# Optimization experiments

Hardware: AMD Instinct MI355X
Metric: run time of the kernel (lower is better)

Reference implementation:

```python
import jax, jax.numpy as jnp
import numpy as np

N, F_IN, UNITS, HEADS = 8192, 256, 64, 4
NEG_BIG = -1e10


def setup_inputs() -> dict:
    key = jax.random.key(0)
    k1, k2, k3, k4, k5 = jax.random.split(key, 5)
    X = jax.random.normal(k1, (N, F_IN), dtype=jnp.float32)
    # sparse-ish binary adjacency with self-loops (float mask, as used by the module)
    A = (jax.random.uniform(k2, (N, N)) < 0.004).astype(jnp.float32)
    A = jnp.maximum(A, jnp.eye(N, dtype=jnp.float32))
    W = jax.random.normal(k3, (HEADS, F_IN, UNITS), dtype=jnp.float32) * (1.0 / np.sqrt(F_IN))
    attn_self = jax.random.normal(k4, (HEADS, UNITS), dtype=jnp.float32) * (1.0 / np.sqrt(UNITS))
    attn_neigh = jax.random.normal(k5, (HEADS, UNITS), dtype=jnp.float32) * (1.0 / np.sqrt(UNITS))
    return {"X": X, "A": A, "W": W, "attn_self": attn_self, "attn_neigh": attn_neigh}


def reference(X, A, W, attn_self, attn_neigh):
    # per-head linear projection: [H, N, U]
    feats = jnp.einsum('nf,hfu->hnu', X, W)
    a_self = jnp.einsum('hnu,hu->hn', feats, attn_self)    # [H, N]
    a_neigh = jnp.einsum('hnu,hu->hn', feats, attn_neigh)  # [H, N]
    # additive GAT scores: e_ij = a_self_i + a_neigh_j -> [H, N, N]
    scores = a_self[:, :, None] + a_neigh[:, None, :]
    scores = jax.nn.leaky_relu(scores, negative_slope=0.2)
    scores = scores + NEG_BIG * (1.0 - A)  # additive mask on non-edges
    attn = jax.nn.softmax(scores, axis=-1)
    # dropout is identity at training=False (module default)
    out = jnp.einsum('hnm,hmu->hnu', attn, feats)  # [H, N, U]
    # 'concat' reduction: head-major concat along feature dim -> [N, H*U]
    out = jnp.transpose(out, (1, 0, 2)).reshape(N, HEADS * UNITS)
    return jax.nn.elu(out)
```

## Files before the change

### kernel.cpp

```cpp
#include <hip/hip_runtime.h>

#define NN    8192
#define FIN   256
#define UNITS 64
#define HEADS 4
#define CTOT  256
#define CAP   256
#define PBLK  512

__global__ __launch_bounds__(256) void k_proj_scan(const float* __restrict__ X,
                                                   const float* __restrict__ W,
                                                   const float* __restrict__ atts,
                                                   const float* __restrict__ attn,
                                                   const float* __restrict__ A,
                                                   float* __restrict__ feats,
                                                   float* __restrict__ s_self,
                                                   float* __restrict__ s_neigh,
                                                   int*   __restrict__ ej_g,
                                                   int*   __restrict__ cnt_g) {
    const int tid = threadIdx.x;
    const int bid = blockIdx.x;

    if (bid >= PBLK) {
        __shared__ int ej[CAP];
        __shared__ int cnt;
        const int i = bid - PBLK;
        if (tid == 0) cnt = 0;
        __syncthreads();
        {
            const float4* Arow4 = reinterpret_cast<const float4*>(A + (size_t)i * NN);
            unsigned mask = 0;
            #pragma unroll
            for (int q = 0; q < 8; ++q) {
                const float4 v = Arow4[q * 256 + tid];
                mask |= (v.x != 0.f ? 1u : 0u) << (4 * q);
                mask |= (v.y != 0.f ? 1u : 0u) << (4 * q + 1);
                mask |= (v.z != 0.f ? 1u : 0u) << (4 * q + 2);
                mask |= (v.w != 0.f ? 1u : 0u) << (4 * q + 3);
            }
            const int c = __popc(mask);
            int base = 0;
            if (c) base = atomicAdd(&cnt, c);
            while (mask) {
                const int b = __ffs(mask) - 1;
                mask &= mask - 1;
                if (base < CAP) ej[base] = (b >> 2) * 1024 + tid * 4 + (b & 3);
                ++base;
            }
        }
        __syncthreads();
        const int ne = min(cnt, CAP);
        if (tid < ne) ej_g[(size_t)i * CAP + tid] = ej[tid];
        if (tid == 0) cnt_g[i] = ne;
        return;
    }

    __shared__ float Xt[32 * 68];
    __shared__ float Wl[32 * 68];
    __shared__ float reds[64];
    __shared__ float redn[64];
    const int rt = bid & 127;
    const int h  = bid >> 7;
    const int r0 = rt * 64;

    const int r  = (tid & 15) * 4;
    const int cl = (tid >> 4) * 4;
    const int srow = tid >> 2;
    const int skq  = (tid & 3) * 8;
    const int wk   = tid >> 3;
    const int wu   = (tid & 7) * 8;

    if (tid < 64) { reds[tid] = 0.f; redn[tid] = 0.f; }

    float acc[4][4];
    #pragma unroll
    for (int a = 0; a < 4; ++a)
        #pragma unroll
        for (int b = 0; b < 4; ++b) acc[a][b] = 0.f;

    for (int k0 = 0; k0 < FIN; k0 += 32) {
        __syncthreads();
        {
            const float4* xp = reinterpret_cast<const float4*>(
                X + (size_t)(r0 + srow) * FIN + k0 + skq);
            const float4 x0 = xp[0], x1 = xp[1];
            const float xs[8] = {x0.x, x0.y, x0.z, x0.w, x1.x, x1.y, x1.z, x1.w};
            #pragma unroll
            for (int m = 0; m < 8; ++m) Xt[(skq + m) * 68 + srow] = xs[m];
        }
        {
            const float4* wp = reinterpret_cast<const float4*>(
                W + (size_t)h * (FIN * UNITS) + (size_t)(k0 + wk) * UNITS + wu);
            const float4 w0 = wp[0], w1 = wp[1];
            const float ws8[8] = {w0.x, w0.y, w0.z, w0.w, w1.x, w1.y, w1.z, w1.w};
            #pragma unroll
            for (int m = 0; m < 8; ++m) Wl[wk * 68 + wu + m] = ws8[m];
        }
        __syncthreads();
        #pragma unroll 8
        for (int k = 0; k < 32; ++k) {
            const float4 a4 = *reinterpret_cast<const float4*>(&Xt[k * 68 + r]);
            const float4 b4 = *reinterpret_cast<const float4*>(&Wl[k * 68 + cl]);
            const float av[4] = {a4.x, a4.y, a4.z, a4.w};
            const float bv[4] = {b4.x, b4.y, b4.z, b4.w};
            #pragma unroll
            for (int ri = 0; ri < 4; ++ri)
                #pragma unroll
                for (int ci = 0; ci < 4; ++ci)
                    acc[ri][ci] += av[ri] * bv[ci];
        }
    }

    float as4[4], an4[4];
    #pragma unroll
    for (int ci = 0; ci < 4; ++ci) {
        as4[ci] = atts[h * UNITS + cl + ci];
        an4[ci] = attn[h * UNITS + cl + ci];
    }
    #pragma unroll
    for (int ri = 0; ri < 4; ++ri) {
        float4 o = make_float4(acc[ri][0], acc[ri][1], acc[ri][2], acc[ri][3]);
        *reinterpret_cast<float4*>(&feats[(size_t)(r0 + r + ri) * CTOT + h * UNITS + cl]) = o;
        const float ps = acc[ri][0] * as4[0] + acc[ri][1] * as4[1]
                       + acc[ri][2] * as4[2] + acc[ri][3] * as4[3];
        const float pn = acc[ri][0] * an4[0] + acc[ri][1] * an4[1]
                       + acc[ri][2] * an4[2] + acc[ri][3] * an4[3];
        atomicAdd(&reds[r + ri], ps);
        atomicAdd(&redn[r + ri], pn);
    }
    __syncthreads();
    if (tid < 64) {
        s_self [((size_t)(r0 + tid) << 2) + h] = reds[tid];
        s_neigh[((size_t)(r0 + tid) << 2) + h] = redn[tid];
    }
}

__global__ __launch_bounds__(256) void k_gat(const int*   __restrict__ ej_g,
                                             const int*   __restrict__ cnt_g,
                                             const float* __restrict__ feats,
                                             const float* __restrict__ s_self,
                                             const float* __restrict__ s_neigh,
                                             float* __restrict__ out) {
    __shared__ int   ej[CAP];
    __shared__ float sc[HEADS][CAP];
    __shared__ float part[HEADS][CTOT];
    __shared__ float rls[HEADS];
    const int tid = threadIdx.x;
    const int i   = blockIdx.x;
    const int ne  = cnt_g[i];
    if (tid < ne) ej[tid] = ej_g[(size_t)i * CAP + tid];
    __syncthreads();

    const int w    = tid >> 6;
    const int lane = tid & 63;
    const float si = s_self[((size_t)i << 2) + w];
    float m = -3.0e38f;
    for (int jj = lane; jj < ne; jj += 64) {
        const int j = ej[jj];
        float e = si + s_neigh[((size_t)j << 2) + w];
        e = (e > 0.f) ? e : 0.2f * e;
        sc[w][jj] = e;
        m = fmaxf(m, e);
    }
    #pragma unroll
    for (int off = 32; off > 0; off >>= 1) m = fmaxf(m, __shfl_xor(m, off, 64));
    float l = 0.f;
    for (int jj = lane; jj < ne; jj += 64) {
        const float p = __expf(sc[w][jj] - m);
        sc[w][jj] = p;
        l += p;
    }
    #pragma unroll
    for (int off = 32; off > 0; off >>= 1) l += __shfl_xor(l, off, 64);
    if (lane == 0) rls[w] = 1.f / l;
    __syncthreads();

    const int h4 = lane >> 4;
    float4 o = make_float4(0.f, 0.f, 0.f, 0.f);
    int jj = w;
    for (; jj + 4 < ne; jj += 8) {
        const int ja = ej[jj], jb = ej[jj + 4];
        const float pa = sc[h4][jj], pb = sc[h4][jj + 4];
        const float4 fa = *reinterpret_cast<const float4*>(
            &feats[(size_t)ja * CTOT + 4 * lane]);
        const float4 fc = *reinterpret_cast<const float4*>(
            &feats[(size_t)jb * CTOT + 4 * lane]);
        o.x += pa * fa.x + pb * fc.x;
        o.y += pa * fa.y + pb * fc.y;
        o.z += pa * fa.z + pb * fc.z;
        o.w += pa * fa.w + pb * fc.w;
    }
    if (jj < ne) {
        const int ja = ej[jj];
        const float pa = sc[h4][jj];
        const float4 fa = *reinterpret_cast<const float4*>(
            &feats[(size_t)ja * CTOT + 4 * lane]);
        o.x += pa * fa.x; o.y += pa * fa.y; o.z += pa * fa.z; o.w += pa * fa.w;
    }
    *reinterpret_cast<float4*>(&part[w][4 * lane]) = o;
    __syncthreads();

    const int c = tid;
    float s = part[0][c] + part[1][c] + part[2][c] + part[3][c];
    s *= rls[c >> 6];
    const float rr = (s > 0.f) ? s : (__expf(s) - 1.f);
    out[(size_t)i * CTOT + c] = rr;
}

extern "C" void kernel_launch(void* const* d_in, const int* in_sizes, int n_in,
                              void* d_out, int out_size, void* d_ws, size_t ws_size,
                              hipStream_t stream) {
    const float* X    = (const float*)d_in[0];
    const float* A    = (const float*)d_in[1];
    const float* W    = (const float*)d_in[2];
    const float* atts = (const float*)d_in[3];
    const float* attn = (const float*)d_in[4];

    float* feats   = (float*)d_ws;
    float* s_self  = feats  + (size_t)NN * CTOT;
    float* s_neigh = s_self + (size_t)NN * HEADS;
    int*   cnt_g   = (int*)(s_neigh + (size_t)NN * HEADS);
    int*   ej_g    = cnt_g + NN;

    k_proj_scan<<<PBLK + NN, 256, 0, stream>>>(X, W, atts, attn, A,
                                               feats, s_self, s_neigh, ej_g, cnt_g);
    k_gat<<<NN, 256, 0, stream>>>(ej_g, cnt_g, feats, s_self, s_neigh, (float*)d_out);
}
```

Measured before the change: 393.8 us.

## Fuse projection, adjacency scan and attention into one cooperative persistent kernel

Replaces the two-kernel launch with a single cooperative kernel of 1024 persistent blocks. The first 512 blocks run the projection GEMM and then scan fewer adjacency rows, while the rest scan more rows, which balances the load. A grid-wide sync follows, after which each block handles 8 rows of softmax aggregation. This removes one launch and overlaps the projection with the A scan, at the cost of a grid barrier, fewer blocks for latency hiding, and a dependence on cooperative launch residency (with the old path as fallback).

Measured after the change: 732.5 us. 86.0% more time.

```diff
diff --git a/kernel.cpp b/kernel.cpp
--- a/kernel.cpp
+++ b/kernel.cpp
@@ -1,4 +1,7 @@
 #include <hip/hip_runtime.h>
+#include <hip/hip_cooperative_groups.h>
+
+namespace cg = cooperative_groups;
 
 #define NN    8192
 #define FIN   256
@@ -6,8 +9,211 @@
 #define HEADS 4
 #define CTOT  256
 #define CAP   256
+
+#define GRID  1024
+#define GBLK  512
+#define RA1   6
+#define RA2   10
+#define RB    8
+
+__global__ __launch_bounds__(256, 4) void k_fused(
+    const float* __restrict__ X,    const float* __restrict__ W,
+    const float* __restrict__ atts, const float* __restrict__ attn,
+    const float* __restrict__ A,
+    float* __restrict__ feats, float* __restrict__ s_self, float* __restrict__ s_neigh,
+    int*   __restrict__ ej_g,  int*   __restrict__ cnt_g,
+    float* __restrict__ out)
+{
+    __shared__ float Xt[32 * 68];
+    __shared__ float Wl[32 * 68];
+    __shared__ float reds[64], redn[64];
+    __shared__ int   ej[CAP];
+    __shared__ int   cnt;
+    __shared__ float sc[HEADS][CAP];
+    __shared__ float part[HEADS][CTOT];
+    __shared__ float rls[HEADS];
+
+    const int tid = threadIdx.x;
+    const int bid = blockIdx.x;
+
+    if (bid < GBLK) {
+        const int rt = bid & 127;
+        const int h  = bid >> 7;
+        const int r0 = rt * 64;
+
+        const int r  = (tid & 15) * 4;
+        const int cl = (tid >> 4) * 4;
+        const int srow = tid >> 2;
+        const int skq  = (tid & 3) * 8;
+        const int wk   = tid >> 3;
+        const int wu   = (tid & 7) * 8;
+
+        if (tid < 64) { reds[tid] = 0.f; redn[tid] = 0.f; }
+
+        float acc[4][4];
+        #pragma unroll
+        for (int a = 0; a < 4; ++a)
+            #pragma unroll
+            for (int b = 0; b < 4; ++b) acc[a][b] = 0.f;
+
+        for (int k0 = 0; k0 < FIN; k0 += 32) {
+            __syncthreads();
+            {
+                const float4* xp = reinterpret_cast<const float4*>(
+                    X + (size_t)(r0 + srow) * FIN + k0 + skq);
+                const float4 x0 = xp[0], x1 = xp[1];
+                const float xs[8] = {x0.x, x0.y, x0.z, x0.w, x1.x, x1.y, x1.z, x1.w};
+                #pragma unroll
+                for (int m = 0; m < 8; ++m) Xt[(skq + m) * 68 + srow] = xs[m];
+            }
+            {
+                const float4* wp = reinterpret_cast<const float4*>(
+                    W + (size_t)h * (FIN * UNITS) + (size_t)(k0 + wk) * UNITS + wu);
+                const float4 w0 = wp[0], w1 = wp[1];
+                const float ws8[8] = {w0.x, w0.y, w0.z, w0.w, w1.x, w1.y, w1.z, w1.w};
+                #pragma unroll
+                for (int m = 0; m < 8; ++m) Wl[wk * 68 + wu + m] = ws8[m];
+            }
+            __syncthreads();
+            #pragma unroll 8
+            for (int k = 0; k < 32; ++k) {
+                const float4 a4 = *reinterpret_cast<const float4*>(&Xt[k * 68 + r]);
+                const float4 b4 = *reinterpret_cast<const float4*>(&Wl[k * 68 + cl]);
+                const float av[4] = {a4.x, a4.y, a4.z, a4.w};
+                const float bv[4] = {b4.x, b4.y, b4.z, b4.w};
+                #pragma unroll
+                for (int ri = 0; ri < 4; ++ri)
+                    #pragma unroll
+                    for (int ci = 0; ci < 4; ++ci)
+                        acc[ri][ci] += av[ri] * bv[ci];
+            }
+        }
+
+        float as4[4], an4[4];
+        #pragma unroll
+        for (int ci = 0; ci < 4; ++ci) {
+            as4[ci] = atts[h * UNITS + cl + ci];
+            an4[ci] = attn[h * UNITS + cl + ci];
+        }
+        #pragma unroll
+        for (int ri = 0; ri < 4; ++ri) {
+            float4 o = make_float4(acc[ri][0], acc[ri][1], acc[ri][2], acc[ri][3]);
+            *reinterpret_cast<float4*>(&feats[(size_t)(r0 + r + ri) * CTOT + h * UNITS + cl]) = o;
+            const float ps = acc[ri][0] * as4[0] + acc[ri][1] * as4[1]
+                           + acc[ri][2] * as4[2] + acc[ri][3] * as4[3];
+            const float pn = acc[ri][0] * an4[0] + acc[ri][1] * an4[1]
+                           + acc[ri][2] * an4[2] + acc[ri][3] * an4[3];
+            atomicAdd(&reds[r + ri], ps);
+            atomicAdd(&redn[r + ri], pn);
+        }
+        __syncthreads();
+        if (tid < 64) {
+            s_self [((size_t)(r0 + tid) << 2) + h] = reds[tid];
+            s_neigh[((size_t)(r0 + tid) << 2) + h] = redn[tid];
+        }
+    }
+
+    const int row0  = (bid < GBLK) ? bid * RA1 : GBLK * RA1 + (bid - GBLK) * RA2;
+    const int nrows = (bid < GBLK) ? RA1 : RA2;
+    for (int rr = 0; rr < nrows; ++rr) {
+        const int i = row0 + rr;
+        if (tid == 0) cnt = 0;
+        __syncthreads();
+        {
+            const float4* Arow4 = reinterpret_cast<const float4*>(A + (size_t)i * NN);
+            unsigned mask = 0;
+            #pragma unroll
+            for (int q = 0; q < 8; ++q) {
+                const float4 v = Arow4[q * 256 + tid];
+                mask |= (v.x != 0.f ? 1u : 0u) << (4 * q);
+                mask |= (v.y != 0.f ? 1u : 0u) << (4 * q + 1);
+                mask |= (v.z != 0.f ? 1u : 0u) << (4 * q + 2);
+                mask |= (v.w != 0.f ? 1u : 0u) << (4 * q + 3);
+            }
+            const int c = __popc(mask);
+            int base = 0;
+            if (c) base = atomicAdd(&cnt, c);
+            while (mask) {
+                const int b = __ffs(mask) - 1;
+                mask &= mask - 1;
+                if (base < CAP) ej[base] = (b >> 2) * 1024 + tid * 4 + (b & 3);
+                ++base;
+            }
+        }
+        __syncthreads();
+        const int ne = min(cnt, CAP);
+        if (tid < ne) ej_g[(size_t)i * CAP + tid] = ej[tid];
+        if (tid == 0) cnt_g[i] = ne;
+        __syncthreads();
+    }
+
+    __threadfence();
+    cg::this_grid().sync();
+    __threadfence();
+
+    const int w    = tid >> 6;
+    const int lane = tid & 63;
+    const int h4   = lane >> 4;
+    for (int rq = 0; rq < RB; ++rq) {
+        const int i  = bid * RB + rq;
+        const int ne = cnt_g[i];
+        if (tid < ne) ej[tid] = ej_g[(size_t)i * CAP + tid];
+        __syncthreads();
+
+        const float si = s_self[((size_t)i << 2) + w];
+        float m = -3.0e38f;
+        for (int jj = lane; jj < ne; jj += 64) {
+            const int j = ej[jj];
+            float e = si + s_neigh[((size_t)j << 2) + w];
+            e = (e > 0.f) ? e : 0.2f * e;
+            sc[w][jj] = e;
+            m = fmaxf(m, e);
+        }
+        #pragma unroll
+        for (int off = 32; off > 0; off >>= 1) m = fmaxf(m, __shfl_xor(m, off, 64));
+        float l = 0.f;
+        for (int jj = lane; jj < ne; jj += 64) {
+            const float p = __expf(sc[w][jj] - m);
+            sc[w][jj] = p;
+            l += p;
+        }
+        #pragma unroll
+        for (int off = 32; off > 0; off >>= 1) l += __shfl_xor(l, off, 64);
+        if (lane == 0) rls[w] = 1.f / l;
+        __syncthreads();
+
+        float4 o = make_float4(0.f, 0.f, 0.f, 0.f);
+        int jj = w;
+        for (; jj + 4 < ne; jj += 8) {
+            const int ja = ej[jj], jb = ej[jj + 4];
+            const float pa = sc[h4][jj], pb = sc[h4][jj + 4];
+            const float4 fa = *reinterpret_cast<const float4*>(
+                &feats[(size_t)ja * CTOT + 4 * lane]);
+            const float4 fc = *reinterpret_cast<const float4*>(
+                &feats[(size_t)jb * CTOT + 4 * lane]);
+            o.x += pa * fa.x + pb * fc.x;
+            o.y += pa * fa.y + pb * fc.y;
+            o.z += pa * fa.z + pb * fc.z;
+            o.w += pa * fa.w + pb * fc.w;
+        }
+        if (jj < ne) {
+            const int ja = ej[jj];
+            const float pa = sc[h4][jj];
+            const float4 fa = *reinterpret_cast<const float4*>(
+                &feats[(size_t)ja * CTOT + 4 * lane]);
+            o.x += pa * fa.x; o.y += pa * fa.y; o.z += pa * fa.z; o.w += pa * fa.w;
+        }
+        *reinterpret_cast<float4*>(&part[w][4 * lane]) = o;
+        __syncthreads();
+
+        float s = part[0][tid] + part[1][tid] + part[2][tid] + part[3][tid];
+        s *= rls[tid >> 6];
+        out[(size_t)i * CTOT + tid] = (s > 0.f) ? s : (__expf(s) - 1.f);
+        __syncthreads();
+    }
+}
+
 #define PBLK  512
-
 __global__ __launch_bounds__(256) void k_proj_scan(const float* __restrict__ X,
                                                    const float* __restrict__ W,
                                                    const float* __restrict__ atts,
@@ -62,7 +268,6 @@
     const int rt = bid & 127;
     const int h  = bid >> 7;
     const int r0 = rt * 64;
-
     const int r  = (tid & 15) * 4;
     const int cl = (tid >> 4) * 4;
     const int srow = tid >> 2;
@@ -200,11 +405,9 @@
     *reinterpret_cast<float4*>(&part[w][4 * lane]) = o;
     __syncthreads();
 
-    const int c = tid;
-    float s = part[0][c] + part[1][c] + part[2][c] + part[3][c];
-    s *= rls[c >> 6];
-    const float rr = (s > 0.f) ? s : (__expf(s) - 1.f);
-    out[(size_t)i * CTOT + c] = rr;
+    float s = part[0][tid] + part[1][tid] + part[2][tid] + part[3][tid];
+    s *= rls[tid >> 6];
+    out[(size_t)i * CTOT + tid] = (s > 0.f) ? s : (__expf(s) - 1.f);
 }
 
 extern "C" void kernel_launch(void* const* d_in, const int* in_sizes, int n_in,
@@ -221,8 +424,17 @@
     float* s_neigh = s_self + (size_t)NN * HEADS;
     int*   cnt_g   = (int*)(s_neigh + (size_t)NN * HEADS);
     int*   ej_g    = cnt_g + NN;
-
-    k_proj_scan<<<PBLK + NN, 256, 0, stream>>>(X, W, atts, attn, A,
-                                               feats, s_self, s_neigh, ej_g, cnt_g);
-    k_gat<<<NN, 256, 0, stream>>>(ej_g, cnt_g, feats, s_self, s_neigh, (float*)d_out);
+    float* out     = (float*)d_out;
+
+    void* args[] = {(void*)&X, (void*)&W, (void*)&atts, (void*)&attn, (void*)&A,
+                    (void*)&feats, (void*)&s_self, (void*)&s_neigh,
+                    (void*)&ej_g, (void*)&cnt_g, (void*)&out};
+    hipError_t e = hipLaunchCooperativeKernel((const void*)k_fused,
+                                              dim3(GRID), dim3(256),
+                                              args, 0, stream);
+    if (e != hipSuccess) {
+        k_proj_scan<<<PBLK + NN, 256, 0, stream>>>(X, W, atts, attn, A,
+                                                   feats, s_self, s_neigh, ej_g, cnt_g);
+        k_gat<<<NN, 256, 0, stream>>>(ej_g, cnt_g, feats, s_self, s_neigh, out);
+    }
 }
```

## Fuse adjacency row scan into GAT aggregation kernel, drop edge-list round trip

Applied to the files above, without the earlier changes.

The adjacency scan moves out of the projection kernel and into the per-row attention kernel, so each block builds its neighbor list in shared memory directly from A. This removes the global writes and reads of the edge index and count arrays. The cost is that the 256 MB A scan now runs after projection instead of alongside it, which loses the earlier overlap of the scan with the projection GEMM.

Result: no change. 396.7 us (+0.7%).

```diff
diff --git a/kernel.cpp b/kernel.cpp
--- a/kernel.cpp
+++ b/kernel.cpp
@@ -6,59 +6,21 @@
 #define HEADS 4
 #define CTOT  256
 #define CAP   256
-#define PBLK  512
-
-__global__ __launch_bounds__(256) void k_proj_scan(const float* __restrict__ X,
-                                                   const float* __restrict__ W,
-                                                   const float* __restrict__ atts,
-                                                   const float* __restrict__ attn,
-                                                   const float* __restrict__ A,
-                                                   float* __restrict__ feats,
-                                                   float* __restrict__ s_self,
-                                                   float* __restrict__ s_neigh,
-                                                   int*   __restrict__ ej_g,
-                                                   int*   __restrict__ cnt_g) {
-    const int tid = threadIdx.x;
-    const int bid = blockIdx.x;
-
-    if (bid >= PBLK) {
-        __shared__ int ej[CAP];
-        __shared__ int cnt;
-        const int i = bid - PBLK;
-        if (tid == 0) cnt = 0;
-        __syncthreads();
-        {
-            const float4* Arow4 = reinterpret_cast<const float4*>(A + (size_t)i * NN);
-            unsigned mask = 0;
-            #pragma unroll
-            for (int q = 0; q < 8; ++q) {
-                const float4 v = Arow4[q * 256 + tid];
-                mask |= (v.x != 0.f ? 1u : 0u) << (4 * q);
-                mask |= (v.y != 0.f ? 1u : 0u) << (4 * q + 1);
-                mask |= (v.z != 0.f ? 1u : 0u) << (4 * q + 2);
-                mask |= (v.w != 0.f ? 1u : 0u) << (4 * q + 3);
-            }
-            const int c = __popc(mask);
-            int base = 0;
-            if (c) base = atomicAdd(&cnt, c);
-            while (mask) {
-                const int b = __ffs(mask) - 1;
-                mask &= mask - 1;
-                if (base < CAP) ej[base] = (b >> 2) * 1024 + tid * 4 + (b & 3);
-                ++base;
-            }
-        }
-        __syncthreads();
-        const int ne = min(cnt, CAP);
-        if (tid < ne) ej_g[(size_t)i * CAP + tid] = ej[tid];
-        if (tid == 0) cnt_g[i] = ne;
-        return;
-    }
-
+#define GBLK  512
+
+__global__ __launch_bounds__(256) void k_proj(const float* __restrict__ X,
+                                              const float* __restrict__ W,
+                                              const float* __restrict__ atts,
+                                              const float* __restrict__ attn,
+                                              float* __restrict__ feats,
+                                              float* __restrict__ s_self,
+                                              float* __restrict__ s_neigh) {
     __shared__ float Xt[32 * 68];
     __shared__ float Wl[32 * 68];
     __shared__ float reds[64];
     __shared__ float redn[64];
+    const int tid = threadIdx.x;
+    const int bid = blockIdx.x;
     const int rt = bid & 127;
     const int h  = bid >> 7;
     const int r0 = rt * 64;
@@ -135,21 +97,44 @@
     }
 }
 
-__global__ __launch_bounds__(256) void k_gat(const int*   __restrict__ ej_g,
-                                             const int*   __restrict__ cnt_g,
-                                             const float* __restrict__ feats,
-                                             const float* __restrict__ s_self,
-                                             const float* __restrict__ s_neigh,
-                                             float* __restrict__ out) {
+__global__ __launch_bounds__(256) void k_scan_gat(const float* __restrict__ A,
+                                                  const float* __restrict__ feats,
+                                                  const float* __restrict__ s_self,
+                                                  const float* __restrict__ s_neigh,
+                                                  float* __restrict__ out) {
     __shared__ int   ej[CAP];
+    __shared__ int   cnt;
     __shared__ float sc[HEADS][CAP];
     __shared__ float part[HEADS][CTOT];
     __shared__ float rls[HEADS];
     const int tid = threadIdx.x;
     const int i   = blockIdx.x;
-    const int ne  = cnt_g[i];
-    if (tid < ne) ej[tid] = ej_g[(size_t)i * CAP + tid];
-    __syncthreads();
+
+    if (tid == 0) cnt = 0;
+    __syncthreads();
+    {
+        const float4* Arow4 = reinterpret_cast<const float4*>(A + (size_t)i * NN);
+        unsigned mask = 0;
+        #pragma unroll
+        for (int q = 0; q < 8; ++q) {
+            const float4 v = Arow4[q * 256 + tid];
+            mask |= (v.x != 0.f ? 1u : 0u) << (4 * q);
+            mask |= (v.y != 0.f ? 1u : 0u) << (4 * q + 1);
+            mask |= (v.z != 0.f ? 1u : 0u) << (4 * q + 2);
+            mask |= (v.w != 0.f ? 1u : 0u) << (4 * q + 3);
+        }
+        const int c = __popc(mask);
+        int base = 0;
+        if (c) base = atomicAdd(&cnt, c);
+        while (mask) {
+            const int b = __ffs(mask) - 1;
+            mask &= mask - 1;
+            if (base < CAP) ej[base] = (b >> 2) * 1024 + tid * 4 + (b & 3);
+            ++base;
+        }
+    }
+    __syncthreads();
+    const int ne = min(cnt, CAP);
 
     const int w    = tid >> 6;
     const int lane = tid & 63;
@@ -200,11 +185,9 @@
     *reinterpret_cast<float4*>(&part[w][4 * lane]) = o;
     __syncthreads();
 
-    const int c = tid;
-    float s = part[0][c] + part[1][c] + part[2][c] + part[3][c];
-    s *= rls[c >> 6];
-    const float rr = (s > 0.f) ? s : (__expf(s) - 1.f);
-    out[(size_t)i * CTOT + c] = rr;
+    float s = part[0][tid] + part[1][tid] + part[2][tid] + part[3][tid];
+    s *= rls[tid >> 6];
+    out[(size_t)i * CTOT + tid] = (s > 0.f) ? s : (__expf(s) - 1.f);
 }
 
 extern "C" void kernel_launch(void* const* d_in, const int* in_sizes, int n_in,
@@ -219,10 +202,7 @@
     float* feats   = (float*)d_ws;
     float* s_self  = feats  + (size_t)NN * CTOT;
     float* s_neigh = s_self + (size_t)NN * HEADS;
-    int*   cnt_g   = (int*)(s_neigh + (size_t)NN * HEADS);
-    int*   ej_g    = cnt_g + NN;
-
-    k_proj_scan<<<PBLK + NN, 256, 0, stream>>>(X, W, atts, attn, A,
-                                               feats, s_self, s_neigh, ej_g, cnt_g);
-    k_gat<<<NN, 256, 0, stream>>>(ej_g, cnt_g, feats, s_self, s_neigh, (float*)d_out);
+
+    k_proj<<<GBLK, 256, 0, stream>>>(X, W, atts, attn, feats, s_self, s_neigh);
+    k_scan_gat<<<NN, 256, 0, stream>>>(A, feats, s_self, s_neigh, (float*)d_out);
 }
```

## Pipeline adjacency scan with GAT aggregation across three kernel launches

Applied to the files above, without the earlier changes.

Splits the adjacency scan into two halves. The first kernel runs the projection plus the scan of rows 0..4095. The second scans rows 4096..8191 while aggregating rows 0..4095, and the third aggregates the remaining rows. The aim is to overlap the bandwidth-bound A scan with the gather-heavy attention aggregation instead of running them back to back. It adds a third launch and mixes block types with different shared memory needs in one grid, which may lower occupancy.

Result: no change. 394.3 us (+0.1%).

```diff
diff --git a/kernel.cpp b/kernel.cpp
--- a/kernel.cpp
+++ b/kernel.cpp
@@ -6,147 +6,54 @@
 #define HEADS 4
 #define CTOT  256
 #define CAP   256
-#define PBLK  512
-
-__global__ __launch_bounds__(256) void k_proj_scan(const float* __restrict__ X,
-                                                   const float* __restrict__ W,
-                                                   const float* __restrict__ atts,
-                                                   const float* __restrict__ attn,
-                                                   const float* __restrict__ A,
-                                                   float* __restrict__ feats,
-                                                   float* __restrict__ s_self,
-                                                   float* __restrict__ s_neigh,
-                                                   int*   __restrict__ ej_g,
-                                                   int*   __restrict__ cnt_g) {
+#define GBLK  512
+#define HALF  4096
+
+
+__device__ __forceinline__ void scan_row(const float* __restrict__ A, int i,
+                                         int* __restrict__ ej_g,
+                                         int* __restrict__ cnt_g,
+                                         int* ej, int* cnt) {
     const int tid = threadIdx.x;
-    const int bid = blockIdx.x;
-
-    if (bid >= PBLK) {
-        __shared__ int ej[CAP];
-        __shared__ int cnt;
-        const int i = bid - PBLK;
-        if (tid == 0) cnt = 0;
-        __syncthreads();
-        {
-            const float4* Arow4 = reinterpret_cast<const float4*>(A + (size_t)i * NN);
-            unsigned mask = 0;
-            #pragma unroll
-            for (int q = 0; q < 8; ++q) {
-                const float4 v = Arow4[q * 256 + tid];
-                mask |= (v.x != 0.f ? 1u : 0u) << (4 * q);
-                mask |= (v.y != 0.f ? 1u : 0u) << (4 * q + 1);
-                mask |= (v.z != 0.f ? 1u : 0u) << (4 * q + 2);
-                mask |= (v.w != 0.f ? 1u : 0u) << (4 * q + 3);
-            }
-            const int c = __popc(mask);
-            int base = 0;
-            if (c) base = atomicAdd(&cnt, c);
-            while (mask) {
-                const int b = __ffs(mask) - 1;
-                mask &= mask - 1;
-                if (base < CAP) ej[base] = (b >> 2) * 1024 + tid * 4 + (b & 3);
-                ++base;
-            }
-        }
-        __syncthreads();
-        const int ne = min(cnt, CAP);
-        if (tid < ne) ej_g[(size_t)i * CAP + tid] = ej[tid];
-        if (tid == 0) cnt_g[i] = ne;
-        return;
-    }
-
-    __shared__ float Xt[32 * 68];
-    __shared__ float Wl[32 * 68];
-    __shared__ float reds[64];
-    __shared__ float redn[64];
-    const int rt = bid & 127;
-    const int h  = bid >> 7;
-    const int r0 = rt * 64;
-
-    const int r  = (tid & 15) * 4;
-    const int cl = (tid >> 4) * 4;
-    const int srow = tid >> 2;
-    const int skq  = (tid & 3) * 8;
-    const int wk   = tid >> 3;
-    const int wu   = (tid & 7) * 8;
-
-    if (tid < 64) { reds[tid] = 0.f; redn[tid] = 0.f; }
-
-    float acc[4][4];
-    #pragma unroll
-    for (int a = 0; a < 4; ++a)
+    if (tid == 0) *cnt = 0;
+    __syncthreads();
+    {
+        const float4* Arow4 = reinterpret_cast<const float4*>(A + (size_t)i * NN);
+        unsigned mask = 0;
         #pragma unroll
-        for (int b = 0; b < 4; ++b) acc[a][b] = 0.f;
-
-    for (int k0 = 0; k0 < FIN; k0 += 32) {
-        __syncthreads();
-        {
-            const float4* xp = reinterpret_cast<const float4*>(
-                X + (size_t)(r0 + srow) * FIN + k0 + skq);
-            const float4 x0 = xp[0], x1 = xp[1];
-            const float xs[8] = {x0.x, x0.y, x0.z, x0.w, x1.x, x1.y, x1.z, x1.w};
-            #pragma unroll
-            for (int m = 0; m < 8; ++m) Xt[(skq + m) * 68 + srow] = xs[m];
-        }
-        {
-            const float4* wp = reinterpret_cast<const float4*>(
-                W + (size_t)h * (FIN * UNITS) + (size_t)(k0 + wk) * UNITS + wu);
-            const float4 w0 = wp[0], w1 = wp[1];
-            const float ws8[8] = {w0.x, w0.y, w0.z, w0.w, w1.x, w1.y, w1.z, w1.w};
-            #pragma unroll
-            for (int m = 0; m < 8; ++m) Wl[wk * 68 + wu + m] = ws8[m];
-        }
-        __syncthreads();
-        #pragma unroll 8
-        for (int k = 0; k < 32; ++k) {
-            const float4 a4 = *reinterpret_cast<const float4*>(&Xt[k * 68 + r]);
-            const float4 b4 = *reinterpret_cast<const float4*>(&Wl[k * 68 + cl]);
-            const float av[4] = {a4.x, a4.y, a4.z, a4.w};
-            const float bv[4] = {b4.x, b4.y, b4.z, b4.w};
-            #pragma unroll
-            for (int ri = 0; ri < 4; ++ri)
-                #pragma unroll
-                for (int ci = 0; ci < 4; ++ci)
-                    acc[ri][ci] += av[ri] * bv[ci];
-        }
-    }
-
-    float as4[4], an4[4];
-    #pragma unroll
-    for (int ci = 0; ci < 4; ++ci) {
-        as4[ci] = atts[h * UNITS + cl + ci];
-        an4[ci] = attn[h * UNITS + cl + ci];
-    }
-    #pragma unroll
-    for (int ri = 0; ri < 4; ++ri) {
-        float4 o = make_float4(acc[ri][0], acc[ri][1], acc[ri][2], acc[ri][3]);
-        *reinterpret_cast<float4*>(&feats[(size_t)(r0 + r + ri) * CTOT + h * UNITS + cl]) = o;
-        const float ps = acc[ri][0] * as4[0] + acc[ri][1] * as4[1]
-                       + acc[ri][2] * as4[2] + acc[ri][3] * as4[3];
-        const float pn = acc[ri][0] * an4[0] + acc[ri][1] * an4[1]
-                       + acc[ri][2] * an4[2] + acc[ri][3] * an4[3];
-        atomicAdd(&reds[r + ri], ps);
-        atomicAdd(&redn[r + ri], pn);
-    }
-    __syncthreads();
-    if (tid < 64) {
-        s_self [((size_t)(r0 + tid) << 2) + h] = reds[tid];
-        s_neigh[((size_t)(r0 + tid) << 2) + h] = redn[tid];
-    }
-}
-
-__global__ __launch_bounds__(256) void k_gat(const int*   __restrict__ ej_g,
-                                             const int*   __restrict__ cnt_g,
-                                             const float* __restrict__ feats,
-                                             const float* __restrict__ s_self,
-                                             const float* __restrict__ s_neigh,
-                                             float* __restrict__ out) {
-    __shared__ int   ej[CAP];
-    __shared__ float sc[HEADS][CAP];
-    __shared__ float part[HEADS][CTOT];
-    __shared__ float rls[HEADS];
+        for (int q = 0; q < 8; ++q) {
+            const float4 v = Arow4[q * 256 + tid];
+            mask |= (v.x != 0.f ? 1u : 0u) << (4 * q);
+            mask |= (v.y != 0.f ? 1u : 0u) << (4 * q + 1);
+            mask |= (v.z != 0.f ? 1u : 0u) << (4 * q + 2);
+            mask |= (v.w != 0.f ? 1u : 0u) << (4 * q + 3);
+        }
+        const int c = __popc(mask);
+        int base = 0;
+        if (c) base = atomicAdd(cnt, c);
+        while (mask) {
+            const int b = __ffs(mask) - 1;
+            mask &= mask - 1;
+            if (base < CAP) ej[base] = (b >> 2) * 1024 + tid * 4 + (b & 3);
+            ++base;
+        }
+    }
+    __syncthreads();
+    const int ne = min(*cnt, CAP);
+    if (tid < ne) ej_g[(size_t)i * CAP + tid] = ej[tid];
+    if (tid == 0) cnt_g[i] = ne;
+}
+
+__device__ __forceinline__ void gat_row(int i,
+                                        const int* __restrict__ ej_g,
+                                        const int* __restrict__ cnt_g,
+                                        const float* __restrict__ feats,
+                                        const float* __restrict__ s_self,
+                                        const float* __restrict__ s_neigh,
+                                        float* __restrict__ out,
+                                        int* ej, float (*sc)[CAP],
+                                        float (*part)[CTOT], float* rls) {
     const int tid = threadIdx.x;
-    const int i   = blockIdx.x;
     const int ne  = cnt_g[i];
     if (tid < ne) ej[tid] = ej_g[(size_t)i * CAP + tid];
     __syncthreads();
@@ -200,11 +107,147 @@
     *reinterpret_cast<float4*>(&part[w][4 * lane]) = o;
     __syncthreads();
 
-    const int c = tid;
-    float s = part[0][c] + part[1][c] + part[2][c] + part[3][c];
-    s *= rls[c >> 6];
-    const float rr = (s > 0.f) ? s : (__expf(s) - 1.f);
-    out[(size_t)i * CTOT + c] = rr;
+    float s = part[0][tid] + part[1][tid] + part[2][tid] + part[3][tid];
+    s *= rls[tid >> 6];
+    out[(size_t)i * CTOT + tid] = (s > 0.f) ? s : (__expf(s) - 1.f);
+}
+
+__global__ __launch_bounds__(256) void k_pipe1(const float* __restrict__ X,
+                                               const float* __restrict__ W,
+                                               const float* __restrict__ atts,
+                                               const float* __restrict__ attn,
+                                               const float* __restrict__ A,
+                                               float* __restrict__ feats,
+                                               float* __restrict__ s_self,
+                                               float* __restrict__ s_neigh,
+                                               int*   __restrict__ ej_g,
+                                               int*   __restrict__ cnt_g) {
+    const int tid = threadIdx.x;
+    const int bid = blockIdx.x;
+
+    if (bid >= GBLK) {
+        __shared__ int ej[CAP];
+        __shared__ int cnt;
+        scan_row(A, bid - GBLK, ej_g, cnt_g, ej, &cnt);
+        return;
+    }
+
+    __shared__ float Xt[32 * 68];
+    __shared__ float Wl[32 * 68];
+    __shared__ float reds[64];
+    __shared__ float redn[64];
+    const int rt = bid & 127;
+    const int h  = bid >> 7;
+    const int r0 = rt * 64;
+
+    const int r  = (tid & 15) * 4;
+    const int cl = (tid >> 4) * 4;
+    const int srow = tid >> 2;
+    const int skq  = (tid & 3) * 8;
+    const int wk   = tid >> 3;
+    const int wu   = (tid & 7) * 8;
+
+    if (tid < 64) { reds[tid] = 0.f; redn[tid] = 0.f; }
+
+    float acc[4][4];
+    #pragma unroll
+    for (int a = 0; a < 4; ++a)
+        #pragma unroll
+        for (int b = 0; b < 4; ++b) acc[a][b] = 0.f;
+
+    for (int k0 = 0; k0 < FIN; k0 += 32) {
+        __syncthreads();
+        {
+            const float4* xp = reinterpret_cast<const float4*>(
+                X + (size_t)(r0 + srow) * FIN + k0 + skq);
+            const float4 x0 = xp[0], x1 = xp[1];
+            const float xs[8] = {x0.x, x0.y, x0.z, x0.w, x1.x, x1.y, x1.z, x1.w};
+            #pragma unroll
+            for (int m = 0; m < 8; ++m) Xt[(skq + m) * 68 + srow] = xs[m];
+        }
+        {
+            const float4* wp = reinterpret_cast<const float4*>(
+                W + (size_t)h * (FIN * UNITS) + (size_t)(k0 + wk) * UNITS + wu);
+            const float4 w0 = wp[0], w1 = wp[1];
+            const float ws8[8] = {w0.x, w0.y, w0.z, w0.w, w1.x, w1.y, w1.z, w1.w};
+            #pragma unroll
+            for (int m = 0; m < 8; ++m) Wl[wk * 68 + wu + m] = ws8[m];
+        }
+        __syncthreads();
+        #pragma unroll 8
+        for (int k = 0; k < 32; ++k) {
+            const float4 a4 = *reinterpret_cast<const float4*>(&Xt[k * 68 + r]);
+            const float4 b4 = *reinterpret_cast<const float4*>(&Wl[k * 68 + cl]);
+            const float av[4] = {a4.x, a4.y, a4.z, a4.w};
+            const float bv[4] = {b4.x, b4.y, b4.z, b4.w};
+            #pragma unroll
+            for (int ri = 0; ri < 4; ++ri)
+                #pragma unroll
+                for (int ci = 0; ci < 4; ++ci)
+                    acc[ri][ci] += av[ri] * bv[ci];
+        }
+    }
+
+    float as4[4], an4[4];
+    #pragma unroll
+    for (int ci = 0; ci < 4; ++ci) {
+        as4[ci] = atts[h * UNITS + cl + ci];
+        an4[ci] = attn[h * UNITS + cl + ci];
+    }
+    #pragma unroll
+    for (int ri = 0; ri < 4; ++ri) {
+        float4 o = make_float4(acc[ri][0], acc[ri][1], acc[ri][2], acc[ri][3]);
+        *reinterpret_cast<float4*>(&feats[(size_t)(r0 + r + ri) * CTOT + h * UNITS + cl]) = o;
+        const float ps = acc[ri][0] * as4[0] + acc[ri][1] * as4[1]
+                       + acc[ri][2] * as4[2] + acc[ri][3] * as4[3];
+        const float pn = acc[ri][0] * an4[0] + acc[ri][1] * an4[1]
+                       + acc[ri][2] * an4[2] + acc[ri][3] * an4[3];
+        atomicAdd(&reds[r + ri], ps);
+        atomicAdd(&redn[r + ri], pn);
+    }
+    __syncthreads();
+    if (tid < 64) {
+        s_self [((size_t)(r0 + tid) << 2) + h] = reds[tid];
+        s_neigh[((size_t)(r0 + tid) << 2) + h] = redn[tid];
+    }
+}
+
+__global__ __launch_bounds__(256) void k_pipe2(const float* __restrict__ A,
+                                               const int*   __restrict__ ej_g_ro,
+                                               const int*   __restrict__ cnt_g_ro,
+                                               int*   __restrict__ ej_g,
+                                               int*   __restrict__ cnt_g,
+                                               const float* __restrict__ feats,
+                                               const float* __restrict__ s_self,
+                                               const float* __restrict__ s_neigh,
+                                               float* __restrict__ out) {
+    const int bid = blockIdx.x;
+    if (bid < HALF) {
+        __shared__ int ej[CAP];
+        __shared__ int cnt;
+        scan_row(A, HALF + bid, ej_g, cnt_g, ej, &cnt);
+    } else {
+        __shared__ int   ej[CAP];
+        __shared__ float sc[HEADS][CAP];
+        __shared__ float part[HEADS][CTOT];
+        __shared__ float rls[HEADS];
+        gat_row(bid - HALF, ej_g_ro, cnt_g_ro, feats, s_self, s_neigh, out,
+                ej, sc, part, rls);
+    }
+}
+
+__global__ __launch_bounds__(256) void k_pipe3(const int*   __restrict__ ej_g,
+                                               const int*   __restrict__ cnt_g,
+                                               const float* __restrict__ feats,
+                                               const float* __restrict__ s_self,
+                                               const float* __restrict__ s_neigh,
+                                               float* __restrict__ out) {
+    __shared__ int   ej[CAP];
+    __shared__ float sc[HEADS][CAP];
+    __shared__ float part[HEADS][CTOT];
+    __shared__ float rls[HEADS];
+    gat_row(HALF + (int)blockIdx.x, ej_g, cnt_g, feats, s_self, s_neigh, out,
+            ej, sc, part, rls);
 }
 
 extern "C" void kernel_launch(void* const* d_in, const int* in_sizes, int n_in,
@@ -221,8 +264,11 @@
     float* s_neigh = s_self + (size_t)NN * HEADS;
     int*   cnt_g   = (int*)(s_neigh + (size_t)NN * HEADS);
     int*   ej_g    = cnt_g + NN;
-
-    k_proj_scan<<<PBLK + NN, 256, 0, stream>>>(X, W, atts, attn, A,
-                                               feats, s_self, s_neigh, ej_g, cnt_g);
-    k_gat<<<NN, 256, 0, stream>>>(ej_g, cnt_g, feats, s_self, s_neigh, (float*)d_out);
-}
+    float* out     = (float*)d_out;
+
+    k_pipe1<<<GBLK + HALF, 256, 0, stream>>>(X, W, atts, attn, A,
+                                             feats, s_self, s_neigh, ej_g, cnt_g);
+    k_pipe2<<<NN, 256, 0, stream>>>(A, ej_g, cnt_g, ej_g, cnt_g,
+                                    feats, s_self, s_neigh, out);
+    k_pipe3<<<HALF, 256, 0, stream>>>(ej_g, cnt_g, feats, s_self, s_neigh, out);
+}
```
